# Performance work log

Hardware: AMD Instinct MI355X
Metric: run time of the kernel (lower is better)

Reference implementation:

```python
import jax, jax.numpy as jnp
import numpy as np

N, C, H, W = 16, 128, 112, 112
P, HG, WG = 98, 16, 16  # 98 patches, 16x16 sample grid each


def setup_inputs() -> dict:
    key = jax.random.key(0)
    k1, k2 = jax.random.split(key)
    feature_maps = jax.random.normal(k1, (N, C, H, W), dtype=jnp.float32)
    # grid_sample normalized coords in [-1, 1]
    meshgrid = jax.random.uniform(k2, (N, P, HG, WG, 2), dtype=jnp.float32) * 2.0 - 1.0
    return {"feature_maps": feature_maps, "meshgrid": meshgrid}


def _grid_sample_bilinear_border(fm, grid):
    # fm: [N, C, H, W]; grid: [N, P, Hg, Wg, 2] (x, y) in [-1, 1]
    # torch grid_sample(mode='bilinear', padding_mode='border', align_corners=False)
    n, c, h, w = fm.shape
    gx, gy = grid[..., 0], grid[..., 1]
    # unnormalize (align_corners=False) then clamp to border
    x = jnp.clip((gx + 1.0) * (w * 0.5) - 0.5, 0.0, w - 1.0)
    y = jnp.clip((gy + 1.0) * (h * 0.5) - 0.5, 0.0, h - 1.0)
    x0 = jnp.floor(x)
    y0 = jnp.floor(y)
    wx = x - x0  # [N, P, Hg, Wg]
    wy = y - y0
    x0i = jnp.clip(x0.astype(jnp.int32), 0, w - 1)
    x1i = jnp.clip(x0i + 1, 0, w - 1)
    y0i = jnp.clip(y0.astype(jnp.int32), 0, h - 1)
    y1i = jnp.clip(y0i + 1, 0, h - 1)
    b = jnp.arange(n).reshape(n, 1, 1, 1)
    gather = lambda yi, xi: fm[b, :, yi, xi]  # -> [N, P, Hg, Wg, C]
    out = (gather(y0i, x0i) * ((1.0 - wy) * (1.0 - wx))[..., None]
           + gather(y0i, x1i) * ((1.0 - wy) * wx)[..., None]
           + gather(y1i, x0i) * (wy * (1.0 - wx))[..., None]
           + gather(y1i, x1i) * (wy * wx)[..., None])
    # [N, P, Hg, Wg, C] -> [N, P, C, Hg, Wg]
    return jnp.moveaxis(out, -1, 2)


def reference(feature_maps, meshgrid):
    # Single fused batched sample over all 98 patches (equivalent to the
    # torch loop of 98 grid_sample calls + stack + permute(1,0,2,3,4)).
    return _grid_sample_bilinear_border(feature_maps, meshgrid)
```

## Files before the change

### kernel.cpp

```cpp
#include <hip/hip_runtime.h>


#define NN 16
#define CC 128
#define HH 112
#define WW 112
#define PP 98
#define PTS 256
#define NPTS (PP * PTS)
#define HWs (HH * WW)
#define THREADS 512

__global__ __launch_bounds__(THREADS) void patches_kernel(
    const float* __restrict__ fm,
    const float* __restrict__ grid,
    float* __restrict__ out) {
  __shared__ float plane[HWs];

  const int c = blockIdx.x;
  const int n = blockIdx.y;
  const int t = threadIdx.x;

  const float4* __restrict__ src =
      reinterpret_cast<const float4*>(fm + ((size_t)n * CC + c) * HWs);
  float4* dst = reinterpret_cast<float4*>(plane);
#pragma unroll
  for (int i = t; i < HWs / 4; i += THREADS) dst[i] = src[i];
  __syncthreads();

  const float2* __restrict__ g =
      reinterpret_cast<const float2*>(grid) + (size_t)n * NPTS;
  float* __restrict__ ob = out + ((size_t)n * PP * CC + c) * PTS;

#pragma unroll 7
  for (int pt = t; pt < NPTS; pt += THREADS) {
    const float2 gg = g[pt];

    float x = fminf(fmaxf(fmaf(gg.x, (float)WW * 0.5f, (float)WW * 0.5f - 0.5f),
                          0.0f), (float)(WW - 1));
    float y = fminf(fmaxf(fmaf(gg.y, (float)HH * 0.5f, (float)HH * 0.5f - 0.5f),
                          0.0f), (float)(HH - 1));

    const float x0f = floorf(x), y0f = floorf(y);
    const float wx = x - x0f, wy = y - y0f;
    const int x0 = (int)x0f;
    const int y0 = (int)y0f;
    const int x1 = min(x0 + 1, WW - 1);
    const int y1 = min(y0 + 1, HH - 1);

    const float w00 = (1.0f - wy) * (1.0f - wx);
    const float w01 = (1.0f - wy) * wx;
    const float w10 = wy * (1.0f - wx);
    const float w11 = wy * wx;

    float v = plane[y0 * WW + x0] * w00;
    v = fmaf(plane[y0 * WW + x1], w01, v);
    v = fmaf(plane[y1 * WW + x0], w10, v);
    v = fmaf(plane[y1 * WW + x1], w11, v);

    const int p = pt >> 8;
    const int s = pt & 255;
    __builtin_nontemporal_store(v, &ob[(size_t)p * CC * PTS + s]);
  }
}

extern "C" void kernel_launch(void* const* d_in, const int* in_sizes, int n_in,
                              void* d_out, int out_size, void* d_ws, size_t ws_size,
                              hipStream_t stream) {
  const float* fm = (const float*)d_in[0];
  const float* grid = (const float*)d_in[1];
  float* out = (float*)d_out;

  dim3 grd(CC, NN);
  dim3 blk(THREADS);
  patches_kernel<<<grd, blk, 0, stream>>>(fm, grid, out);
}
```

Before: 294.3 us.

## Precompute per-point sample offsets and weights in a separate table kernel

Adds a prepass kernel that converts each grid coordinate into a byte offset plus fractional weights and stores them as int4 in the workspace. The main kernel, which recomputes these per channel, then reads the table instead, so the coordinate math runs once per point rather than 128 times. The shared plane is padded with zeros so the neighbour clamps can be dropped, and the loop now uses a fixed trip count with simplified store addressing. In exchange each channel block reads 16 bytes per point instead of 8 and there is an extra kernel launch. If no workspace is available it falls back to the old path.

```diff
diff --git a/kernel.cpp b/kernel.cpp
--- a/kernel.cpp
+++ b/kernel.cpp
@@ -9,13 +9,36 @@
 #define PTS 256
 #define NPTS (PP * PTS)
 #define HWs (HH * WW)
+#define PAD 113
 #define THREADS 512
+#define TOTPTS (NN * NPTS)
+#define TAB_BYTES ((size_t)TOTPTS * 16)
 
+__global__ __launch_bounds__(256) void precompute_kernel(
+    const float* __restrict__ grid, int4* __restrict__ tab) {
+  const int i = blockIdx.x * 256 + threadIdx.x;
+  const float2 g = reinterpret_cast<const float2*>(grid)[i];
+  const float x = fminf(fmaxf(fmaf(g.x, (float)WW * 0.5f, (float)WW * 0.5f - 0.5f),
+                              0.0f), (float)(WW - 1));
+  const float y = fminf(fmaxf(fmaf(g.y, (float)HH * 0.5f, (float)HH * 0.5f - 0.5f),
+                              0.0f), (float)(HH - 1));
+  const float x0f = floorf(x), y0f = floorf(y);
+  const int x0 = (int)x0f, y0 = (int)y0f;
+  int4 e;
+  e.x = (y0 * WW + x0) * 4;
+  e.y = __float_as_int(x - x0f);
+  e.z = __float_as_int(y - y0f);
+  e.w = 0;
+  tab[i] = e;
+}
+
+template <bool USE_TAB>
 __global__ __launch_bounds__(THREADS) void patches_kernel(
     const float* __restrict__ fm,
     const float* __restrict__ grid,
+    const int4* __restrict__ tab,
     float* __restrict__ out) {
-  __shared__ float plane[HWs];
+  __shared__ float plane[HWs + PAD];
 
   const int c = blockIdx.x;
   const int n = blockIdx.y;
@@ -24,43 +47,54 @@
   const float4* __restrict__ src =
       reinterpret_cast<const float4*>(fm + ((size_t)n * CC + c) * HWs);
   float4* dst = reinterpret_cast<float4*>(plane);
-#pragma unroll
   for (int i = t; i < HWs / 4; i += THREADS) dst[i] = src[i];
+  if (t < PAD) plane[HWs + t] = 0.0f;
   __syncthreads();
 
-  const float2* __restrict__ g =
-      reinterpret_cast<const float2*>(grid) + (size_t)n * NPTS;
-  float* __restrict__ ob = out + ((size_t)n * PP * CC + c) * PTS;
+  float* __restrict__ ob = out + ((size_t)n * PP * CC + c) * PTS
+                               + (size_t)(t >> 8) * CC * PTS + (t & 255);
 
+  if (USE_TAB) {
+    const int4* __restrict__ tb = tab + (size_t)n * NPTS;
 #pragma unroll 7
-  for (int pt = t; pt < NPTS; pt += THREADS) {
-    const float2 gg = g[pt];
-
-    float x = fminf(fmaxf(fmaf(gg.x, (float)WW * 0.5f, (float)WW * 0.5f - 0.5f),
-                          0.0f), (float)(WW - 1));
-    float y = fminf(fmaxf(fmaf(gg.y, (float)HH * 0.5f, (float)HH * 0.5f - 0.5f),
-                          0.0f), (float)(HH - 1));
-
-    const float x0f = floorf(x), y0f = floorf(y);
-    const float wx = x - x0f, wy = y - y0f;
-    const int x0 = (int)x0f;
-    const int y0 = (int)y0f;
-    const int x1 = min(x0 + 1, WW - 1);
-    const int y1 = min(y0 + 1, HH - 1);
-
-    const float w00 = (1.0f - wy) * (1.0f - wx);
-    const float w01 = (1.0f - wy) * wx;
-    const float w10 = wy * (1.0f - wx);
-    const float w11 = wy * wx;
-
-    float v = plane[y0 * WW + x0] * w00;
-    v = fmaf(plane[y0 * WW + x1], w01, v);
-    v = fmaf(plane[y1 * WW + x0], w10, v);
-    v = fmaf(plane[y1 * WW + x1], w11, v);
-
-    const int p = pt >> 8;
-    const int s = pt & 255;
-    __builtin_nontemporal_store(v, &ob[(size_t)p * CC * PTS + s]);
+    for (int it = 0; it < NPTS / THREADS; ++it) {
+      const int4 e = tb[t + it * THREADS];
+      const float wx = __int_as_float(e.y);
+      const float wy = __int_as_float(e.z);
+      const float* p0 = reinterpret_cast<const float*>(
+          reinterpret_cast<const char*>(plane) + e.x);
+      const float v00 = p0[0], v01 = p0[1];
+      const float v10 = p0[WW], v11 = p0[WW + 1];
+      const float ux = 1.0f - wx, uy = 1.0f - wy;
+      float v = v00 * (uy * ux);
+      v = fmaf(v01, uy * wx, v);
+      v = fmaf(v10, wy * ux, v);
+      v = fmaf(v11, wy * wx, v);
+      __builtin_nontemporal_store(v, ob + (size_t)it * 2 * CC * PTS);
+    }
+  } else {
+    const float2* __restrict__ g =
+        reinterpret_cast<const float2*>(grid) + (size_t)n * NPTS;
+#pragma unroll 7
+    for (int it = 0; it < NPTS / THREADS; ++it) {
+      const float2 gg = g[t + it * THREADS];
+      const float x = fminf(fmaxf(fmaf(gg.x, (float)WW * 0.5f, (float)WW * 0.5f - 0.5f),
+                                  0.0f), (float)(WW - 1));
+      const float y = fminf(fmaxf(fmaf(gg.y, (float)HH * 0.5f, (float)HH * 0.5f - 0.5f),
+                                  0.0f), (float)(HH - 1));
+      const float x0f = floorf(x), y0f = floorf(y);
+      const float wx = x - x0f, wy = y - y0f;
+      const int o00 = (int)y0f * WW + (int)x0f;
+      const float* p0 = plane + o00;
+      const float v00 = p0[0], v01 = p0[1];
+      const float v10 = p0[WW], v11 = p0[WW + 1];
+      const float ux = 1.0f - wx, uy = 1.0f - wy;
+      float v = v00 * (uy * ux);
+      v = fmaf(v01, uy * wx, v);
+      v = fmaf(v10, wy * ux, v);
+      v = fmaf(v11, wy * wx, v);
+      __builtin_nontemporal_store(v, ob + (size_t)it * 2 * CC * PTS);
+    }
   }
 }
 
@@ -71,7 +105,14 @@
   const float* grid = (const float*)d_in[1];
   float* out = (float*)d_out;
 
+  const bool use_tab = (d_ws != nullptr) && (ws_size >= TAB_BYTES);
   dim3 grd(CC, NN);
   dim3 blk(THREADS);
-  patches_kernel<<<grd, blk, 0, stream>>>(fm, grid, out);
+  if (use_tab) {
+    int4* tab = (int4*)d_ws;
+    precompute_kernel<<<TOTPTS / 256, 256, 0, stream>>>(grid, tab);
+    patches_kernel<true><<<grd, blk, 0, stream>>>(fm, grid, tab, out);
+  } else {
+    patches_kernel<false><<<grd, blk, 0, stream>>>(fm, grid, nullptr, out);
+  }
 }
```

New measurement: 301.9 us. 2.6% more time.

## Pack two channels as fp16 pairs in shared memory per block

Applied to the files above, without the earlier changes.

Each block now handles two channels. Both planes are stored in LDS as packed half2 values, so one LDS read returns a sample for both channels, and the grid coordinates and weights are computed once for the two outputs. This halves the grid reads and the index math per output and cuts LDS reads per output. The cost is fp16 rounding of the feature values, which may exceed the accuracy tolerance, and half as many blocks (1024). Padding replaces the clamped x1/y1 indices, so edge samples read a neighbouring or zeroed cell that gets zero weight only when wx or wy is exactly 0.

```diff
diff --git a/kernel.cpp b/kernel.cpp
--- a/kernel.cpp
+++ b/kernel.cpp
@@ -1,4 +1,5 @@
 #include <hip/hip_runtime.h>
+#include <hip/hip_fp16.h>
 
 
 #define NN 16
@@ -9,58 +10,89 @@
 #define PTS 256
 #define NPTS (PP * PTS)
 #define HWs (HH * WW)
+#define PAD 113
 #define THREADS 512
+
+typedef float f32x4 __attribute__((ext_vector_type(4)));
+typedef unsigned int u32x4 __attribute__((ext_vector_type(4)));
+
+__device__ __forceinline__ unsigned int pack2(float a, float b) {
+  __half2 h = __floats2half2_rn(a, b);
+  return *reinterpret_cast<unsigned int*>(&h);
+}
+
+__device__ __forceinline__ float2 unpack2(unsigned int q) {
+  __half2 h = *reinterpret_cast<__half2*>(&q);
+  return __half22float2(h);
+}
 
 __global__ __launch_bounds__(THREADS) void patches_kernel(
     const float* __restrict__ fm,
     const float* __restrict__ grid,
     float* __restrict__ out) {
-  __shared__ float plane[HWs];
+  __shared__ unsigned int plane[HWs + PAD];
 
-  const int c = blockIdx.x;
+  const int cp = blockIdx.x;
   const int n = blockIdx.y;
   const int t = threadIdx.x;
+  const int c0 = cp * 2;
 
-  const float4* __restrict__ src =
-      reinterpret_cast<const float4*>(fm + ((size_t)n * CC + c) * HWs);
-  float4* dst = reinterpret_cast<float4*>(plane);
-#pragma unroll
-  for (int i = t; i < HWs / 4; i += THREADS) dst[i] = src[i];
+  const f32x4* __restrict__ srcA =
+      reinterpret_cast<const f32x4*>(fm + ((size_t)n * CC + c0) * HWs);
+  const f32x4* __restrict__ srcB =
+      reinterpret_cast<const f32x4*>(fm + ((size_t)n * CC + c0 + 1) * HWs);
+  u32x4* dst = reinterpret_cast<u32x4*>(plane);
+  for (int i = t; i < HWs / 4; i += THREADS) {
+    const f32x4 a = __builtin_nontemporal_load(&srcA[i]);
+    const f32x4 b = __builtin_nontemporal_load(&srcB[i]);
+    u32x4 q;
+    q.x = pack2(a.x, b.x);
+    q.y = pack2(a.y, b.y);
+    q.z = pack2(a.z, b.z);
+    q.w = pack2(a.w, b.w);
+    dst[i] = q;
+  }
+  if (t < PAD) plane[HWs + t] = 0u;
   __syncthreads();
 
   const float2* __restrict__ g =
       reinterpret_cast<const float2*>(grid) + (size_t)n * NPTS;
-  float* __restrict__ ob = out + ((size_t)n * PP * CC + c) * PTS;
+  float* __restrict__ obase = out + ((size_t)n * PP * CC + c0) * PTS;
 
 #pragma unroll 7
-  for (int pt = t; pt < NPTS; pt += THREADS) {
+  for (int it = 0; it < NPTS / THREADS; ++it) {
+    const int pt = t + it * THREADS;
     const float2 gg = g[pt];
 
-    float x = fminf(fmaxf(fmaf(gg.x, (float)WW * 0.5f, (float)WW * 0.5f - 0.5f),
-                          0.0f), (float)(WW - 1));
-    float y = fminf(fmaxf(fmaf(gg.y, (float)HH * 0.5f, (float)HH * 0.5f - 0.5f),
-                          0.0f), (float)(HH - 1));
-
+    const float x = fminf(fmaxf(fmaf(gg.x, (float)WW * 0.5f, (float)WW * 0.5f - 0.5f),
+                                0.0f), (float)(WW - 1));
+    const float y = fminf(fmaxf(fmaf(gg.y, (float)HH * 0.5f, (float)HH * 0.5f - 0.5f),
+                                0.0f), (float)(HH - 1));
     const float x0f = floorf(x), y0f = floorf(y);
     const float wx = x - x0f, wy = y - y0f;
-    const int x0 = (int)x0f;
-    const int y0 = (int)y0f;
-    const int x1 = min(x0 + 1, WW - 1);
-    const int y1 = min(y0 + 1, HH - 1);
 
-    const float w00 = (1.0f - wy) * (1.0f - wx);
-    const float w01 = (1.0f - wy) * wx;
-    const float w10 = wy * (1.0f - wx);
-    const float w11 = wy * wx;
+    const unsigned int* p0 = reinterpret_cast<const unsigned int*>(
+        reinterpret_cast<const char*>(plane) + ((int)y0f * WW + (int)x0f) * 4);
+    const float2 f00 = unpack2(p0[0]);
+    const float2 f01 = unpack2(p0[1]);
+    const float2 f10 = unpack2(p0[WW]);
+    const float2 f11 = unpack2(p0[WW + 1]);
 
-    float v = plane[y0 * WW + x0] * w00;
-    v = fmaf(plane[y0 * WW + x1], w01, v);
-    v = fmaf(plane[y1 * WW + x0], w10, v);
-    v = fmaf(plane[y1 * WW + x1], w11, v);
+    const float ux = 1.0f - wx, uy = 1.0f - wy;
+    const float w00 = uy * ux, w01 = uy * wx, w10 = wy * ux, w11 = wy * wx;
 
-    const int p = pt >> 8;
-    const int s = pt & 255;
-    __builtin_nontemporal_store(v, &ob[(size_t)p * CC * PTS + s]);
+    float vA = f00.x * w00;
+    vA = fmaf(f01.x, w01, vA);
+    vA = fmaf(f10.x, w10, vA);
+    vA = fmaf(f11.x, w11, vA);
+    float vB = f00.y * w00;
+    vB = fmaf(f01.y, w01, vB);
+    vB = fmaf(f10.y, w10, vB);
+    vB = fmaf(f11.y, w11, vB);
+
+    float* o = obase + (size_t)(pt >> 8) * CC * PTS + (pt & 255);
+    __builtin_nontemporal_store(vA, o);
+    __builtin_nontemporal_store(vB, o + PTS);
   }
 }
 
@@ -71,7 +103,7 @@
   const float* grid = (const float*)d_in[1];
   float* out = (float*)d_out;
 
-  dim3 grd(CC, NN);
+  dim3 grd(CC / 2, NN);
   dim3 blk(THREADS);
   patches_kernel<<<grd, blk, 0, stream>>>(fm, grid, out);
 }
```

After: 281.8 us. 4.3% less time.
